# Optimization experiments

Measured on AMD Instinct MI355X. Metric: run time of the kernel, lower is better.

Reference implementation:

```python
import jax, jax.numpy as jnp
import numpy as np

BOS_IDX = 1


def setup_inputs() -> dict:
    key = jax.random.key(0)
    ks = jax.random.split(key, 12)
    B, T, S, H, L, V = 16, 128, 64, 512, 2, 32000
    s = 0.05
    return {
        "encoder_outputs": jax.random.normal(ks[0], (B, S, H), jnp.float32),
        "encoder_h": jax.random.normal(ks[1], (L, B, H), jnp.float32) * s,
        "encoder_c": jax.random.normal(ks[2], (L, B, H), jnp.float32) * s,
        "target_tensor": jax.random.randint(ks[3], (B, T), 0, V),
        "embedding": jax.random.normal(ks[4], (V, H), jnp.float32) * s,
        "W_ih": jax.random.normal(ks[5], (L, 4 * H, H), jnp.float32) * s,
        "W_hh": jax.random.normal(ks[6], (L, 4 * H, H), jnp.float32) * s,
        "b_ih": jax.random.normal(ks[7], (L, 4 * H), jnp.float32) * s,
        "b_hh": jax.random.normal(ks[8], (L, 4 * H), jnp.float32) * s,
        "W_out": jax.random.normal(ks[9], (V, H), jnp.float32) * s,
        "b_out": jax.random.normal(ks[10], (V,), jnp.float32) * s,
    }


def reference(encoder_outputs, encoder_h, encoder_c, target_tensor,
              embedding, W_ih, W_hh, b_ih, b_hh, W_out, b_out):
    B, T = target_tensor.shape
    L = W_ih.shape[0]
    # Teacher-forced inputs: BOS then target[:, :-1]
    tokens = jnp.concatenate(
        [jnp.full((B, 1), BOS_IDX, dtype=target_tensor.dtype),
         target_tensor[:, :-1]], axis=1)  # [B, T]
    x = jax.nn.relu(embedding[tokens])  # [B, T, H]
    # The original loop resets (h, c) to encoder_states at EVERY step, so all
    # T single-step LSTM cells are independent -> vectorize over T.
    h_last, c_last = [], []
    for l in range(L):
        h0 = encoder_h[l]  # [B, H]
        c0 = encoder_c[l][:, None, :]  # [B, 1, H]
        gates = (jnp.einsum('bth,gh->btg', x, W_ih[l]) + b_ih[l]
                 + (jnp.einsum('bh,gh->bg', h0, W_hh[l]) + b_hh[l])[:, None, :])
        i, f, g, o = jnp.split(gates, 4, axis=-1)  # torch gate order i,f,g,o
        c = jax.nn.sigmoid(f) * c0 + jax.nn.sigmoid(i) * jnp.tanh(g)
        h = jax.nn.sigmoid(o) * jnp.tanh(c)  # [B, T, H]
        h_last.append(h[:, -1, :])
        c_last.append(c[:, -1, :])
        x = h  # input to next layer (dropout=0 / eval)
    logits = jnp.einsum('bth,vh->btv', x, W_out) + b_out  # [B, T, V]
    return logits, (jnp.stack(h_last), jnp.stack(c_last))
```

## Files before the change

kernel.cpp:

```cpp
#include <hip/hip_runtime.h>
#include <hip/hip_bf16.h>

typedef __bf16 bf16_t;
typedef __bf16 bf16x8 __attribute__((ext_vector_type(8)));
typedef __bf16 bf16x4 __attribute__((ext_vector_type(4)));
typedef float f32x4 __attribute__((ext_vector_type(4)));

#define B_ 16
#define T_ 128
#define H_ 512
#define L_ 2
#define V_ 32000
#define G_ 2048
#define M_ 2048

#define BM 128
#define BN 128
#define BK 32

__global__ __launch_bounds__(256) void cvt_bf16(const float* __restrict__ in,
                                                bf16_t* __restrict__ out) {
    int idx = blockIdx.x * 256 + threadIdx.x;
    float4 v = ((const float4*)in)[idx];
    bf16x4 o;
    o[0] = (bf16_t)v.x; o[1] = (bf16_t)v.y; o[2] = (bf16_t)v.z; o[3] = (bf16_t)v.w;
    ((bf16x4*)out)[idx] = o;
}

__global__ __launch_bounds__(256) void embed_relu(const float* __restrict__ emb,
                                                  const int* __restrict__ target,
                                                  bf16_t* __restrict__ x) {
    int idx = blockIdx.x * 256 + threadIdx.x;
    int m  = idx >> 7;
    int h4 = (idx & 127) << 2;
    int b = m >> 7, t = m & 127;
    int tok = (t == 0) ? 1 : target[b * T_ + t - 1];
    float4 v = *(const float4*)(emb + (size_t)tok * H_ + h4);
    bf16x4 o;
    o[0] = (bf16_t)fmaxf(v.x, 0.f);
    o[1] = (bf16_t)fmaxf(v.y, 0.f);
    o[2] = (bf16_t)fmaxf(v.z, 0.f);
    o[3] = (bf16_t)fmaxf(v.w, 0.f);
    *(bf16x4*)(x + (size_t)m * H_ + h4) = o;
}

__global__ __launch_bounds__(256) void hproj_kernel(const float* __restrict__ enc_h,
                                                    const float* __restrict__ W_hh,
                                                    const float* __restrict__ b_ih,
                                                    const float* __restrict__ b_hh,
                                                    float* __restrict__ biasall) {
    int idx = blockIdx.x * 256 + threadIdx.x;
    int b = idx & 15;
    int g = (idx >> 4) & (G_ - 1);
    int l = idx >> 15;
    const float* hrow = enc_h + ((size_t)l * B_ + b) * H_;
    const float* wrow = W_hh + ((size_t)l * G_ + g) * H_;
    float acc = b_ih[l * G_ + g] + b_hh[l * G_ + g];
    #pragma unroll 4
    for (int k = 0; k < H_; k += 4) {
        float4 hv = *(const float4*)(hrow + k);
        float4 wv = *(const float4*)(wrow + k);
        acc += hv.x * wv.x + hv.y * wv.y + hv.z * wv.z + hv.w * wv.w;
    }
    biasall[((size_t)l * B_ + b) * G_ + g] = acc;
}

__global__ __launch_bounds__(256) void gemm_bt(const bf16_t* __restrict__ A,
                                               const bf16_t* __restrict__ B,
                                               float* __restrict__ C,
                                               const float* __restrict__ bias,
                                               int M, int N, int K, int bias_mode) {
    __shared__ __align__(16) bf16_t As[BM * BK];
    __shared__ __align__(16) bf16_t Bs[BN * BK];

    const int tid  = threadIdx.x;
    const int lane = tid & 63;
    const int wave = tid >> 6;
    const int wm = wave >> 1, wn = wave & 1;
    const int quad = lane >> 4;
    const int r16  = lane & 15;

    const int tileM = blockIdx.x * BM;
    const int tileN = blockIdx.y * BN;

    const int srow = lane >> 2;
    const int scol = (lane & 3) * 8;

    f32x4 acc[4][4];
    #pragma unroll
    for (int i = 0; i < 4; i++)
        #pragma unroll
        for (int j = 0; j < 4; j++) acc[i][j] = (f32x4){0.f, 0.f, 0.f, 0.f};

    const int nk = K / BK;
    for (int kt = 0; kt < nk; ++kt) {
        const int k0 = kt * BK;
        #pragma unroll
        for (int j = 0; j < 2; ++j) {
            const int r0 = j * 64 + wave * 16;
            const bf16_t* ga = A + (size_t)(tileM + r0 + srow) * K + k0 + scol;
            const bf16_t* gb = B + (size_t)(tileN + r0 + srow) * K + k0 + scol;
            __builtin_amdgcn_global_load_lds(
                (const __attribute__((address_space(1))) void*)ga,
                (__attribute__((address_space(3))) void*)(As + r0 * BK), 16, 0, 0);
            __builtin_amdgcn_global_load_lds(
                (const __attribute__((address_space(1))) void*)gb,
                (__attribute__((address_space(3))) void*)(Bs + r0 * BK), 16, 0, 0);
        }
        __syncthreads();

        bf16x8 af[4], bfr[4];
        #pragma unroll
        for (int mi = 0; mi < 4; mi++)
            af[mi] = *(const bf16x8*)(As + (wm * 64 + mi * 16 + r16) * BK + quad * 8);
        #pragma unroll
        for (int ni = 0; ni < 4; ni++)
            bfr[ni] = *(const bf16x8*)(Bs + (wn * 64 + ni * 16 + r16) * BK + quad * 8);
        #pragma unroll
        for (int mi = 0; mi < 4; mi++)
            #pragma unroll
            for (int ni = 0; ni < 4; ni++)
                acc[mi][ni] = __builtin_amdgcn_mfma_f32_16x16x32_bf16(
                    af[mi], bfr[ni], acc[mi][ni], 0, 0, 0);
        __syncthreads();
    }

    const float* brow = bias_mode ? (bias + (size_t)blockIdx.x * N) : bias;
    #pragma unroll
    for (int mi = 0; mi < 4; mi++) {
        #pragma unroll
        for (int ni = 0; ni < 4; ni++) {
            const int col = tileN + wn * 64 + ni * 16 + r16;
            const float bv = brow[col];
            #pragma unroll
            for (int rr = 0; rr < 4; rr++) {
                const int row = tileM + wm * 64 + mi * 16 + quad * 4 + rr;
                C[(size_t)row * N + col] = acc[mi][ni][rr] + bv;
            }
        }
    }
}

__device__ __forceinline__ float sigf(float x) { return 1.f / (1.f + __expf(-x)); }
__device__ __forceinline__ float tanhf_(float x) { return 2.f / (1.f + __expf(-2.f * x)) - 1.f; }

__global__ __launch_bounds__(256) void lstm_cell(const float* __restrict__ gates,
                                                 const float* __restrict__ enc_c,
                                                 bf16_t* __restrict__ x,
                                                 float* __restrict__ out_h,
                                                 float* __restrict__ out_c,
                                                 int l) {
    int idx = blockIdx.x * 256 + threadIdx.x;
    int m  = idx >> 9;
    int hh = idx & (H_ - 1);
    int b = m >> 7, t = m & 127;
    const float* grow = gates + (size_t)m * G_;
    float gi = grow[hh];
    float gf = grow[H_ + hh];
    float gg = grow[2 * H_ + hh];
    float go = grow[3 * H_ + hh];
    float c0 = enc_c[((size_t)l * B_ + b) * H_ + hh];
    float c = sigf(gf) * c0 + sigf(gi) * tanhf_(gg);
    float h = sigf(go) * tanhf_(c);
    x[idx] = (bf16_t)h;
    if (t == T_ - 1) {
        out_h[((size_t)l * B_ + b) * H_ + hh] = h;
        out_c[((size_t)l * B_ + b) * H_ + hh] = c;
    }
}

extern "C" void kernel_launch(void* const* d_in, const int* in_sizes, int n_in,
                              void* d_out, int out_size, void* d_ws, size_t ws_size,
                              hipStream_t stream) {
    const float* enc_h  = (const float*)d_in[1];
    const float* enc_c  = (const float*)d_in[2];
    const int*   target = (const int*)d_in[3];
    const float* emb    = (const float*)d_in[4];
    const float* W_ih   = (const float*)d_in[5];
    const float* W_hh   = (const float*)d_in[6];
    const float* b_ih   = (const float*)d_in[7];
    const float* b_hh   = (const float*)d_in[8];
    const float* W_out  = (const float*)d_in[9];
    const float* b_out  = (const float*)d_in[10];
    float* out = (float*)d_out;

    char* w = (char*)d_ws;
    bf16_t* x       = (bf16_t*)(w);
    bf16_t* wih_b   = (bf16_t*)(w + 2097152);
    bf16_t* wout_b  = (bf16_t*)(w + 6291456);
    float*  gates   = (float*)(w + 39059456);
    float*  biasall = (float*)(w + 55836672);

    float* out_h = out + (size_t)M_ * V_;
    float* out_c = out_h + (size_t)L_ * B_ * H_;

    cvt_bf16<<<(L_ * G_ * H_) / 1024, 256, 0, stream>>>(W_ih, wih_b);
    cvt_bf16<<<(V_ * H_) / 1024, 256, 0, stream>>>(W_out, wout_b);
    embed_relu<<<(M_ * H_ / 4) / 256, 256, 0, stream>>>(emb, target, x);
    hproj_kernel<<<(L_ * G_ * B_) / 256, 256, 0, stream>>>(enc_h, W_hh, b_ih, b_hh, biasall);

    for (int l = 0; l < L_; ++l) {
        dim3 gg(M_ / BM, G_ / BN);
        gemm_bt<<<gg, 256, 0, stream>>>(x, wih_b + (size_t)l * G_ * H_, gates,
                                        biasall + (size_t)l * B_ * G_, M_, G_, H_, 1);
        lstm_cell<<<(M_ * H_) / 256, 256, 0, stream>>>(gates, enc_c, x, out_h, out_c, l);
    }

    dim3 gl(M_ / BM, V_ / BN);
    gemm_bt<<<gl, 256, 0, stream>>>(x, wout_b, out, b_out, M_, V_, H_, 0);
}
```

Measured before the change: 523.5 us.

## Fuse LSTM cell into gate GEMM epilogue and merge prep kernels

Permutes W_ih rows (and the matching bias entries) so that each 16-column group of a GEMM tile holds the i, f, g and o gates for the same hidden units. This lets the gate GEMM epilogue compute the LSTM cell directly and write h as bf16, so the fp32 gates buffer and separate lstm_cell kernels are no longer needed. The four preprocessing kernels are merged into one launch. In exchange, input and output x buffers are now ping-ponged, and the permuted indexing adds some complexity.

```diff
diff --git a/kernel.cpp b/kernel.cpp
--- a/kernel.cpp
+++ b/kernel.cpp
@@ -18,58 +18,80 @@
 #define BN 128
 #define BK 32
 
-__global__ __launch_bounds__(256) void cvt_bf16(const float* __restrict__ in,
-                                                bf16_t* __restrict__ out) {
-    int idx = blockIdx.x * 256 + threadIdx.x;
-    float4 v = ((const float4*)in)[idx];
-    bf16x4 o;
-    o[0] = (bf16_t)v.x; o[1] = (bf16_t)v.y; o[2] = (bf16_t)v.z; o[3] = (bf16_t)v.w;
-    ((bf16x4*)out)[idx] = o;
-}
-
-__global__ __launch_bounds__(256) void embed_relu(const float* __restrict__ emb,
-                                                  const int* __restrict__ target,
-                                                  bf16_t* __restrict__ x) {
-    int idx = blockIdx.x * 256 + threadIdx.x;
-    int m  = idx >> 7;
-    int h4 = (idx & 127) << 2;
-    int b = m >> 7, t = m & 127;
-    int tok = (t == 0) ? 1 : target[b * T_ + t - 1];
-    float4 v = *(const float4*)(emb + (size_t)tok * H_ + h4);
-    bf16x4 o;
-    o[0] = (bf16_t)fmaxf(v.x, 0.f);
-    o[1] = (bf16_t)fmaxf(v.y, 0.f);
-    o[2] = (bf16_t)fmaxf(v.z, 0.f);
-    o[3] = (bf16_t)fmaxf(v.w, 0.f);
-    *(bf16x4*)(x + (size_t)m * H_ + h4) = o;
-}
-
-__global__ __launch_bounds__(256) void hproj_kernel(const float* __restrict__ enc_h,
-                                                    const float* __restrict__ W_hh,
-                                                    const float* __restrict__ b_ih,
-                                                    const float* __restrict__ b_hh,
-                                                    float* __restrict__ biasall) {
-    int idx = blockIdx.x * 256 + threadIdx.x;
-    int b = idx & 15;
-    int g = (idx >> 4) & (G_ - 1);
-    int l = idx >> 15;
-    const float* hrow = enc_h + ((size_t)l * B_ + b) * H_;
-    const float* wrow = W_hh + ((size_t)l * G_ + g) * H_;
-    float acc = b_ih[l * G_ + g] + b_hh[l * G_ + g];
-    #pragma unroll 4
-    for (int k = 0; k < H_; k += 4) {
-        float4 hv = *(const float4*)(hrow + k);
-        float4 wv = *(const float4*)(wrow + k);
-        acc += hv.x * wv.x + hv.y * wv.y + hv.z * wv.z + hv.w * wv.w;
-    }
-    biasall[((size_t)l * B_ + b) * G_ + g] = acc;
-}
-
-__global__ __launch_bounds__(256) void gemm_bt(const bf16_t* __restrict__ A,
-                                               const bf16_t* __restrict__ B,
-                                               float* __restrict__ C,
-                                               const float* __restrict__ bias,
-                                               int M, int N, int K, int bias_mode) {
+__device__ __forceinline__ float sigf(float x) { return 1.f / (1.f + __expf(-x)); }
+__device__ __forceinline__ float tanhf_(float x) { return 2.f / (1.f + __expf(-2.f * x)) - 1.f; }
+
+__global__ __launch_bounds__(256) void prep_kernel(
+    const float* __restrict__ W_ih, const float* __restrict__ W_out,
+    const float* __restrict__ emb,  const int* __restrict__ target,
+    const float* __restrict__ enc_h, const float* __restrict__ W_hh,
+    const float* __restrict__ b_ih, const float* __restrict__ b_hh,
+    bf16_t* __restrict__ wih_b, bf16_t* __restrict__ wout_b,
+    bf16_t* __restrict__ xa, float* __restrict__ biasall)
+{
+    const int bid = blockIdx.x;
+    const int tid = threadIdx.x;
+
+    if (bid < 2048) {
+        int t = bid * 256 + tid;
+        int l = t >> 18;
+        int r = t & 262143;
+        int rowp = r >> 7;
+        int k  = (r & 127) << 2;
+        int hhblock = rowp >> 6;
+        int gate    = (rowp >> 4) & 3;
+        int hhlocal = rowp & 15;
+        int gorig = gate * H_ + hhblock * 16 + hhlocal;
+        float4 v = *(const float4*)(W_ih + ((size_t)l * G_ + gorig) * H_ + k);
+        bf16x4 o;
+        o[0] = (bf16_t)v.x; o[1] = (bf16_t)v.y; o[2] = (bf16_t)v.z; o[3] = (bf16_t)v.w;
+        *(bf16x4*)(wih_b + ((size_t)l * G_ + rowp) * H_ + k) = o;
+    } else if (bid < 18048) {
+        int t = (bid - 2048) * 256 + tid;
+        float4 v = ((const float4*)W_out)[t];
+        bf16x4 o;
+        o[0] = (bf16_t)v.x; o[1] = (bf16_t)v.y; o[2] = (bf16_t)v.z; o[3] = (bf16_t)v.w;
+        ((bf16x4*)wout_b)[t] = o;
+    } else if (bid < 19072) {
+        int idx = (bid - 18048) * 256 + tid;
+        int m  = idx >> 7;
+        int h4 = (idx & 127) << 2;
+        int b = m >> 7, tt = m & 127;
+        int tok = (tt == 0) ? 1 : target[b * T_ + tt - 1];
+        float4 v = *(const float4*)(emb + (size_t)tok * H_ + h4);
+        bf16x4 o;
+        o[0] = (bf16_t)fmaxf(v.x, 0.f);
+        o[1] = (bf16_t)fmaxf(v.y, 0.f);
+        o[2] = (bf16_t)fmaxf(v.z, 0.f);
+        o[3] = (bf16_t)fmaxf(v.w, 0.f);
+        *(bf16x4*)(xa + (size_t)m * H_ + h4) = o;
+    } else {
+        int idx = (bid - 19072) * 256 + tid;
+        int b = idx & 15;
+        int g = (idx >> 4) & (G_ - 1);
+        int l = idx >> 15;
+        const float* hrow = enc_h + ((size_t)l * B_ + b) * H_;
+        const float* wrow = W_hh + ((size_t)l * G_ + g) * H_;
+        float acc = b_ih[l * G_ + g] + b_hh[l * G_ + g];
+        #pragma unroll 4
+        for (int k = 0; k < H_; k += 4) {
+            float4 hv = *(const float4*)(hrow + k);
+            float4 wv = *(const float4*)(wrow + k);
+            acc += hv.x * wv.x + hv.y * wv.y + hv.z * wv.z + hv.w * wv.w;
+        }
+        int gate = g >> 9;
+        int hh = g & (H_ - 1);
+        int rowp = ((hh >> 4) << 6) + (gate << 4) + (hh & 15);
+        biasall[((size_t)l * B_ + b) * G_ + rowp] = acc;
+    }
+}
+
+__global__ __launch_bounds__(256) void gemm_gates(
+    const bf16_t* __restrict__ A, const bf16_t* __restrict__ Bw,
+    const float* __restrict__ biasL, const float* __restrict__ enc_c,
+    bf16_t* __restrict__ xout, float* __restrict__ out_h, float* __restrict__ out_c,
+    int l)
+{
     __shared__ __align__(16) bf16_t As[BM * BK];
     __shared__ __align__(16) bf16_t Bs[BN * BK];
 
@@ -92,6 +114,94 @@
         #pragma unroll
         for (int j = 0; j < 4; j++) acc[i][j] = (f32x4){0.f, 0.f, 0.f, 0.f};
 
+    for (int kt = 0; kt < H_ / BK; ++kt) {
+        const int k0 = kt * BK;
+        #pragma unroll
+        for (int j = 0; j < 2; ++j) {
+            const int r0 = j * 64 + wave * 16;
+            const bf16_t* ga = A  + (size_t)(tileM + r0 + srow) * H_ + k0 + scol;
+            const bf16_t* gb = Bw + (size_t)(tileN + r0 + srow) * H_ + k0 + scol;
+            __builtin_amdgcn_global_load_lds(
+                (const __attribute__((address_space(1))) void*)ga,
+                (__attribute__((address_space(3))) void*)(As + r0 * BK), 16, 0, 0);
+            __builtin_amdgcn_global_load_lds(
+                (const __attribute__((address_space(1))) void*)gb,
+                (__attribute__((address_space(3))) void*)(Bs + r0 * BK), 16, 0, 0);
+        }
+        __syncthreads();
+
+        bf16x8 af[4], bfr[4];
+        #pragma unroll
+        for (int mi = 0; mi < 4; mi++)
+            af[mi] = *(const bf16x8*)(As + (wm * 64 + mi * 16 + r16) * BK + quad * 8);
+        #pragma unroll
+        for (int ni = 0; ni < 4; ni++)
+            bfr[ni] = *(const bf16x8*)(Bs + (wn * 64 + ni * 16 + r16) * BK + quad * 8);
+        #pragma unroll
+        for (int mi = 0; mi < 4; mi++)
+            #pragma unroll
+            for (int ni = 0; ni < 4; ni++)
+                acc[mi][ni] = __builtin_amdgcn_mfma_f32_16x16x32_bf16(
+                    af[mi], bfr[ni], acc[mi][ni], 0, 0, 0);
+        __syncthreads();
+    }
+
+    const int b = blockIdx.x;
+    const float* brow = biasL + (size_t)b * G_;
+    const int hh = ((tileN + wn * 64) >> 2) + r16;
+    const float c0 = enc_c[((size_t)l * B_ + b) * H_ + hh];
+    float bv[4];
+    #pragma unroll
+    for (int ni = 0; ni < 4; ni++)
+        bv[ni] = brow[tileN + wn * 64 + ni * 16 + r16];
+
+    #pragma unroll
+    for (int mi = 0; mi < 4; mi++) {
+        #pragma unroll
+        for (int rr = 0; rr < 4; rr++) {
+            float vi = acc[mi][0][rr] + bv[0];
+            float vf = acc[mi][1][rr] + bv[1];
+            float vg = acc[mi][2][rr] + bv[2];
+            float vo = acc[mi][3][rr] + bv[3];
+            float cs = sigf(vf) * c0 + sigf(vi) * tanhf_(vg);
+            float h  = sigf(vo) * tanhf_(cs);
+            int row = tileM + wm * 64 + mi * 16 + quad * 4 + rr;
+            xout[(size_t)row * H_ + hh] = (bf16_t)h;
+            if ((row & (T_ - 1)) == T_ - 1) {
+                out_h[((size_t)l * B_ + b) * H_ + hh] = h;
+                out_c[((size_t)l * B_ + b) * H_ + hh] = cs;
+            }
+        }
+    }
+}
+
+__global__ __launch_bounds__(256) void gemm_bt(const bf16_t* __restrict__ A,
+                                               const bf16_t* __restrict__ B,
+                                               float* __restrict__ C,
+                                               const float* __restrict__ bias,
+                                               int M, int N, int K) {
+    __shared__ __align__(16) bf16_t As[BM * BK];
+    __shared__ __align__(16) bf16_t Bs[BN * BK];
+
+    const int tid  = threadIdx.x;
+    const int lane = tid & 63;
+    const int wave = tid >> 6;
+    const int wm = wave >> 1, wn = wave & 1;
+    const int quad = lane >> 4;
+    const int r16  = lane & 15;
+
+    const int tileM = blockIdx.x * BM;
+    const int tileN = blockIdx.y * BN;
+
+    const int srow = lane >> 2;
+    const int scol = (lane & 3) * 8;
+
+    f32x4 acc[4][4];
+    #pragma unroll
+    for (int i = 0; i < 4; i++)
+        #pragma unroll
+        for (int j = 0; j < 4; j++) acc[i][j] = (f32x4){0.f, 0.f, 0.f, 0.f};
+
     const int nk = K / BK;
     for (int kt = 0; kt < nk; ++kt) {
         const int k0 = kt * BK;
@@ -125,47 +235,22 @@
         __syncthreads();
     }
 
-    const float* brow = bias_mode ? (bias + (size_t)blockIdx.x * N) : bias;
+    float bv[4];
+    #pragma unroll
+    for (int ni = 0; ni < 4; ni++)
+        bv[ni] = bias[tileN + wn * 64 + ni * 16 + r16];
+
     #pragma unroll
     for (int mi = 0; mi < 4; mi++) {
         #pragma unroll
         for (int ni = 0; ni < 4; ni++) {
             const int col = tileN + wn * 64 + ni * 16 + r16;
-            const float bv = brow[col];
             #pragma unroll
             for (int rr = 0; rr < 4; rr++) {
                 const int row = tileM + wm * 64 + mi * 16 + quad * 4 + rr;
-                C[(size_t)row * N + col] = acc[mi][ni][rr] + bv;
+                C[(size_t)row * N + col] = acc[mi][ni][rr] + bv[ni];
             }
         }
-    }
-}
-
-__device__ __forceinline__ float sigf(float x) { return 1.f / (1.f + __expf(-x)); }
-__device__ __forceinline__ float tanhf_(float x) { return 2.f / (1.f + __expf(-2.f * x)) - 1.f; }
-
-__global__ __launch_bounds__(256) void lstm_cell(const float* __restrict__ gates,
-                                                 const float* __restrict__ enc_c,
-                                                 bf16_t* __restrict__ x,
-                                                 float* __restrict__ out_h,
-                                                 float* __restrict__ out_c,
-                                                 int l) {
-    int idx = blockIdx.x * 256 + threadIdx.x;
-    int m  = idx >> 9;
-    int hh = idx & (H_ - 1);
-    int b = m >> 7, t = m & 127;
-    const float* grow = gates + (size_t)m * G_;
-    float gi = grow[hh];
-    float gf = grow[H_ + hh];
-    float gg = grow[2 * H_ + hh];
-    float go = grow[3 * H_ + hh];
-    float c0 = enc_c[((size_t)l * B_ + b) * H_ + hh];
-    float c = sigf(gf) * c0 + sigf(gi) * tanhf_(gg);
-    float h = sigf(go) * tanhf_(c);
-    x[idx] = (bf16_t)h;
-    if (t == T_ - 1) {
-        out_h[((size_t)l * B_ + b) * H_ + hh] = h;
-        out_c[((size_t)l * B_ + b) * H_ + hh] = c;
     }
 }
 
@@ -185,27 +270,23 @@
     float* out = (float*)d_out;
 
     char* w = (char*)d_ws;
-    bf16_t* x       = (bf16_t*)(w);
-    bf16_t* wih_b   = (bf16_t*)(w + 2097152);
-    bf16_t* wout_b  = (bf16_t*)(w + 6291456);
-    float*  gates   = (float*)(w + 39059456);
-    float*  biasall = (float*)(w + 55836672);
+    bf16_t* xa      = (bf16_t*)(w);
+    bf16_t* xb      = (bf16_t*)(w + 2097152);
+    bf16_t* wih_b   = (bf16_t*)(w + 4194304);
+    bf16_t* wout_b  = (bf16_t*)(w + 8388608);
+    float*  biasall = (float*)(w + 41156608);
 
     float* out_h = out + (size_t)M_ * V_;
     float* out_c = out_h + (size_t)L_ * B_ * H_;
 
-    cvt_bf16<<<(L_ * G_ * H_) / 1024, 256, 0, stream>>>(W_ih, wih_b);
-    cvt_bf16<<<(V_ * H_) / 1024, 256, 0, stream>>>(W_out, wout_b);
-    embed_relu<<<(M_ * H_ / 4) / 256, 256, 0, stream>>>(emb, target, x);
-    hproj_kernel<<<(L_ * G_ * B_) / 256, 256, 0, stream>>>(enc_h, W_hh, b_ih, b_hh, biasall);
-
-    for (int l = 0; l < L_; ++l) {
-        dim3 gg(M_ / BM, G_ / BN);
-        gemm_bt<<<gg, 256, 0, stream>>>(x, wih_b + (size_t)l * G_ * H_, gates,
-                                        biasall + (size_t)l * B_ * G_, M_, G_, H_, 1);
-        lstm_cell<<<(M_ * H_) / 256, 256, 0, stream>>>(gates, enc_c, x, out_h, out_c, l);
-    }
-
-    dim3 gl(M_ / BM, V_ / BN);
-    gemm_bt<<<gl, 256, 0, stream>>>(x, wout_b, out, b_out, M_, V_, H_, 0);
-}
+    prep_kernel<<<19328, 256, 0, stream>>>(W_ih, W_out, emb, target, enc_h, W_hh,
+                                           b_ih, b_hh, wih_b, wout_b, xa, biasall);
+
+    gemm_gates<<<dim3(M_ / BM, G_ / BN), 256, 0, stream>>>(
+        xa, wih_b, biasall, enc_c, xb, out_h, out_c, 0);
+    gemm_gates<<<dim3(M_ / BM, G_ / BN), 256, 0, stream>>>(
+        xb, wih_b + (size_t)G_ * H_, biasall + (size_t)B_ * G_, enc_c, xa, out_h, out_c, 1);
+
+    gemm_bt<<<dim3(M_ / BM, V_ / BN), 256, 0, stream>>>(
+        xa, wout_b, out, b_out, M_, V_, H_);
+}
```

After: 580.9 us. 1.11x slower.
